# Kernel optimization log

Hardware: AMD Instinct MI355X
Metric: run time of the kernel (lower is better)

Reference implementation:

```python
import jax, jax.numpy as jnp
import numpy as np

OUTPUT_SIZES = [1, 3, 6, 8]  # SPP pyramid -> total KV length 110

def _bounds(n, out):
    # PyTorch AdaptiveMaxPool2d bin boundaries
    return [((i * n) // out, -((-(i + 1) * n) // out)) for i in range(out)]

def adaptive_max_pool2d(x, out):
    # x: [B, C, H, W] -> [B, C, out, out]
    B, C, H, W = x.shape
    rows = jnp.stack([x[:, :, s:e, :].max(axis=2) for s, e in _bounds(H, out)], axis=2)
    return jnp.stack([rows[:, :, :, s:e].max(axis=3) for s, e in _bounds(W, out)], axis=3)

def spp(x):
    # [B, C, H, W] -> [B, C, S] with S = sum(o*o) = 110
    B, C = x.shape[:2]
    return jnp.concatenate(
        [adaptive_max_pool2d(x, o).reshape(B, C, o * o) for o in OUTPUT_SIZES], axis=2)

def conv1x1(x, w):
    # 1x1 conv, no bias: w [O, C], x [B, C, H, W]
    return jnp.einsum('oc,bchw->bohw', w, x)

def setup_inputs() -> dict:
    key = jax.random.key(0)
    ks = jax.random.split(key, 6)
    B, C, H, W = 16, 512, 64, 64
    IC = C // 2
    x = jax.random.normal(ks[0], (B, C, H, W), jnp.float32)
    y = jax.random.normal(ks[1], (B, C, H, W), jnp.float32)
    sc = 1.0 / np.sqrt(C)
    w_phi = jax.random.normal(ks[2], (IC, C), jnp.float32) * sc
    w_theta = jax.random.normal(ks[3], (IC, C), jnp.float32) * sc
    w_g = jax.random.normal(ks[4], (IC, C), jnp.float32) * sc
    w_mask = jax.random.normal(ks[5], (C, IC), jnp.float32) * (1.0 / np.sqrt(IC))
    return {"x": x, "y": y, "w_phi": w_phi, "w_theta": w_theta,
            "w_g": w_g, "w_mask": w_mask}

def reference(x, y, w_phi, w_theta, w_g, w_mask):
    B, C, H, W = x.shape
    IC = w_phi.shape[0]
    N = H * W
    # Query: [B, N, IC]
    x_phi = conv1x1(x, w_phi).reshape(B, IC, N).transpose(0, 2, 1)
    # Keys/values from SPP-pooled y: [B, IC, S] / [B, S, IC]
    y_theta = spp(conv1x1(y, w_theta))
    y_g = spp(conv1x1(y, w_g)).transpose(0, 2, 1)
    # Attention with softmax over the QUERY axis (dim=1), as in the source
    attn = jax.nn.softmax(jnp.einsum('bnc,bcs->bns', x_phi, y_theta), axis=1)
    agg = jnp.einsum('bns,bsc->bnc', attn, y_g)          # [B, N, IC]
    agg = agg.transpose(0, 2, 1).reshape(B, IC, H, W)     # [B, IC, H, W]
    mask = conv1x1(agg, w_mask)                           # [B, C, H, W]
    return mask + x
```

## Files before the change

kernel.cpp:

```cpp
#include <hip/hip_runtime.h>

#define DI __device__ __forceinline__

typedef __attribute__((ext_vector_type(8))) __bf16 bf16x8;
typedef __attribute__((ext_vector_type(4))) float f32x4;

DI unsigned short f2bf(float x) {
  union { float f; unsigned u; } v; v.f = x;
  unsigned r = v.u + 0x7fffu + ((v.u >> 16) & 1u);
  return (unsigned short)(r >> 16);
}
DI float bf2f(unsigned short h) {
  union { unsigned u; float f; } v; v.u = ((unsigned)h) << 16;
  return v.f;
}
DI unsigned pack2(float a, float b) {
  return (unsigned)f2bf(a) | (((unsigned)f2bf(b)) << 16);
}

DI void gl_lds16(const void* g, void* l) {
  __builtin_amdgcn_global_load_lds(
      (const __attribute__((address_space(1))) void*)g,
      (__attribute__((address_space(3))) void*)l, 16, 0, 0);
}

__global__ __launch_bounds__(256) void pw_conv(
    const float* __restrict__ w_theta, const float* __restrict__ w_g,
    unsigned short* __restrict__ wTG)
{
  int e = (blockIdx.x * 256 + threadIdx.x) * 8;
  const float* src = (e < 131072) ? (w_theta + e) : (w_g + (e - 131072));
  float4 a = *(const float4*)src;
  float4 c = *(const float4*)(src + 4);
  uint4 u;
  u.x = pack2(a.x, a.y); u.y = pack2(a.z, a.w);
  u.z = pack2(c.x, c.y); u.w = pack2(c.z, c.w);
  *(uint4*)(wTG + e) = u;
}

__global__ __launch_bounds__(256) void p0_transpose(
    const float* __restrict__ src, unsigned short* __restrict__ dst)
{
  const int n0 = blockIdx.x * 64, c0 = blockIdx.y * 64, b = blockIdx.z;
  const int tid = threadIdx.x;
  __shared__ float T[64 * 65];
  #pragma unroll
  for (int p = 0; p < 4; ++p) {
    int r = p * 16 + (tid >> 4);
    int n4 = (tid & 15) << 2;
    *(float4*)&T[r * 65 + n4] =
        *(const float4*)(src + ((size_t)(b * 512 + c0 + r)) * 4096 + n0 + n4);
  }
  __syncthreads();
  int n = tid >> 2, cc = (tid & 3) * 16;
  unsigned u[8];
  #pragma unroll
  for (int j = 0; j < 16; j += 2)
    u[j >> 1] = pack2(T[(cc + j) * 65 + n], T[(cc + j + 1) * 65 + n]);
  unsigned short* d = dst + ((size_t)(b * 4096 + n0 + n)) * 512 + c0 + cc;
  *(uint4*)(d) = make_uint4(u[0], u[1], u[2], u[3]);
  *(uint4*)(d + 8) = make_uint4(u[4], u[5], u[6], u[7]);
}

__constant__ int c_RS[18] = {0, 0,21,42, 0,10,21,32,42,53, 0,8,16,24,32,40,48,56};
__constant__ int c_RE[18] = {64, 22,43,64, 11,22,32,43,54,64, 8,16,24,32,40,48,56,64};

__global__ __launch_bounds__(256) void k1f_conv_pool(
    const unsigned short* __restrict__ yT, const unsigned short* __restrict__ wTG,
    unsigned short* __restrict__ Rbuf)
{
  const int tid = threadIdx.x;
  const int id = blockIdx.x;
  const int tile = (id & 7) * 16 + (id >> 3);
  const int mb = (tile & 3) * 128;
  const int nbt = tile >> 2;
  const int nb = nbt * 128;
  const int b  = blockIdx.y;
  const int lane = tid & 63, wv = tid >> 6;
  const int wm = (wv & 1) * 64, wn = (wv >> 1) * 64;
  const int l15 = lane & 15, l4 = lane >> 4;

  __shared__ __align__(16) char smem[33280];
  unsigned short* As = (unsigned short*)smem;
  unsigned short* Bs = (unsigned short*)(smem + 8192);
  float* P = (float*)smem;

  f32x4 acc[4][4];
  #pragma unroll
  for (int i = 0; i < 4; ++i)
    #pragma unroll
    for (int j = 0; j < 4; ++j) acc[i][j] = f32x4{0.f, 0.f, 0.f, 0.f};

  for (int kb = 0; kb < 512; kb += 32) {
    #pragma unroll
    for (int p = 0; p < 2; ++p) {
      int chunk = (wv * 2 + p) * 64 + lane;
      int row = chunk >> 2, c16 = chunk & 3;
      gl_lds16(wTG + ((size_t)(mb + row)) * 512 + kb + c16 * 8,
               As + (wv * 2 + p) * 512);
      gl_lds16(yT + ((size_t)(b * 4096 + nb + row)) * 512 + kb + c16 * 8,
               Bs + (wv * 2 + p) * 512);
    }
    __syncthreads();
    bf16x8 af[4], bfr[4];
    #pragma unroll
    for (int i = 0; i < 4; ++i)
      af[i] = *(const bf16x8*)&As[(wm + i * 16 + l15) * 32 + l4 * 8];
    #pragma unroll
    for (int j = 0; j < 4; ++j)
      bfr[j] = *(const bf16x8*)&Bs[(wn + j * 16 + l15) * 32 + l4 * 8];
    #pragma unroll
    for (int i = 0; i < 4; ++i)
      #pragma unroll
      for (int j = 0; j < 4; ++j)
        acc[i][j] = __builtin_amdgcn_mfma_f32_16x16x32_bf16(af[i], bfr[j], acc[i][j], 0, 0, 0);
    __syncthreads();
  }

  const int hloc = wv >> 1;
  #pragma unroll
  for (int pass = 0; pass < 2; ++pass) {
    __syncthreads();
    if (hloc == pass) {
      #pragma unroll
      for (int i = 0; i < 4; ++i)
        #pragma unroll
        for (int j = 0; j < 4; ++j)
          #pragma unroll
          for (int r = 0; r < 4; ++r)
            P[(wm + i * 16 + l4 * 4 + r) * 65 + j * 16 + l15] = acc[i][j][r];
    }
    __syncthreads();
    const int o = tid & 127;
    size_t rbase = (((size_t)(b * 64 + nbt * 2 + pass)) * 18) * 512 + mb + o;
    if (tid < 128) {
      float b0 = -3.4e38f, b1 = b0, b2 = b0, b3 = b0;
      #pragma unroll
      for (int w = 0; w < 64; ++w) {
        float v = P[o * 65 + w];
        b0 = fmaxf(b0, v);
        if (w < 22) b1 = fmaxf(b1, v);
        if (w >= 21 && w < 43) b2 = fmaxf(b2, v);
        if (w >= 42) b3 = fmaxf(b3, v);
      }
      Rbuf[rbase]           = f2bf(b0);
      Rbuf[rbase + 512]     = f2bf(b1);
      Rbuf[rbase + 2 * 512] = f2bf(b2);
      Rbuf[rbase + 3 * 512] = f2bf(b3);
    } else {
      float s6[6], s8[8];
      #pragma unroll
      for (int i = 0; i < 6; ++i) s6[i] = -3.4e38f;
      #pragma unroll
      for (int i = 0; i < 8; ++i) s8[i] = -3.4e38f;
      constexpr int R6S[6] = {0, 10, 21, 32, 42, 53};
      constexpr int R6E[6] = {11, 22, 32, 43, 54, 64};
      #pragma unroll
      for (int w = 0; w < 64; ++w) {
        float v = P[o * 65 + w];
        #pragma unroll
        for (int i = 0; i < 6; ++i)
          if (w >= R6S[i] && w < R6E[i]) s6[i] = fmaxf(s6[i], v);
        s8[w >> 3] = fmaxf(s8[w >> 3], v);
      }
      #pragma unroll
      for (int i = 0; i < 6; ++i) Rbuf[rbase + (size_t)(4 + i) * 512] = f2bf(s6[i]);
      #pragma unroll
      for (int i = 0; i < 8; ++i) Rbuf[rbase + (size_t)(10 + i) * 512] = f2bf(s8[i]);
    }
  }
}

__global__ __launch_bounds__(256) void k2_pool_final(
    const unsigned short* __restrict__ Rbuf, float* __restrict__ Pt,
    float* __restrict__ Pg)
{
  const int s = blockIdx.x, b = blockIdx.y, tid = threadIdx.x;
  size_t obase = ((size_t)(b * 128) + s) * 256 + tid;
  if (s >= 110) { Pt[obase] = 0.f; Pg[obase] = 0.f; return; }
  int he, wb;
  if (s == 0)      { he = 0; wb = 0; }
  else if (s < 10) { int i = s - 1;  he = 1 + i / 3;  wb = 1 + i % 3; }
  else if (s < 46) { int i = s - 10; he = 4 + i / 6;  wb = 4 + i % 6; }
  else             { int i = s - 46; he = 10 + i / 8; wb = 10 + i % 8; }
  float m0 = -3.4e38f, m1 = -3.4e38f;
  int e = c_RE[he];
  for (int h = c_RS[he]; h < e; ++h) {
    const unsigned short* r = Rbuf + (((size_t)(b * 64 + h)) * 18 + wb) * 512;
    m0 = fmaxf(m0, bf2f(r[tid]));
    m1 = fmaxf(m1, bf2f(r[tid + 256]));
  }
  Pt[obase] = m0;
  Pg[obase] = m1;
}

__global__ __launch_bounds__(256) void k3_fused(
    const float* __restrict__ Pt, const float* __restrict__ Pg,
    const float* __restrict__ w_phi, const float* __restrict__ w_mask,
    unsigned short* __restrict__ Kth, unsigned short* __restrict__ Ktl,
    unsigned short* __restrict__ Vb)
{
  __shared__ __align__(16) char sm3[51200];
  const int tid = threadIdx.x;
  const int tx = tid & 15, ty = tid >> 4;
  const int b = blockIdx.y;
  if (blockIdx.z == 0) {
    const int ct = blockIdx.x;
    const int c0 = tx * 4, s0 = ty * 8;
    float* Ls = (float*)sm3;
    float* Ws = Ls + 128 * 64;
    float acc[8][4] = {};
    for (int kc = 0; kc < 256; kc += 64) {
      #pragma unroll
      for (int j = 0; j < 8; ++j) {
        int flat = tid + 256 * j;
        int row = flat >> 4, k4 = (flat & 15) << 2;
        *(float4*)&Ls[row * 64 + k4] =
            *(const float4*)(Pt + ((size_t)(b * 128) + row) * 256 + kc + k4);
      }
      #pragma unroll
      for (int j = 0; j < 4; ++j) {
        int flat = tid + 256 * j;
        int row = flat >> 4, c4 = (flat & 15) << 2;
        *(float4*)&Ws[row * 68 + c4] =
            *(const float4*)(w_phi + (size_t)(kc + row) * 512 + ct * 64 + c4);
      }
      __syncthreads();
      for (int k = 0; k < 64; k += 4) {
        float4 wv[4];
        #pragma unroll
        for (int kk = 0; kk < 4; ++kk) wv[kk] = *(const float4*)&Ws[(k + kk) * 68 + c0];
        #pragma unroll
        for (int i = 0; i < 8; ++i) {
          float4 a = *(const float4*)&Ls[(s0 + i) * 64 + k];
          const float* ap = (const float*)&a;
          #pragma unroll
          for (int kk = 0; kk < 4; ++kk) {
            const float* wp = (const float*)&wv[kk];
            acc[i][0] += ap[kk] * wp[0];
            acc[i][1] += ap[kk] * wp[1];
            acc[i][2] += ap[kk] * wp[2];
            acc[i][3] += ap[kk] * wp[3];
          }
        }
      }
      __syncthreads();
    }
    #pragma unroll
    for (int i = 0; i < 8; ++i) {
      unsigned short hi[4]; float lo[4];
      #pragma unroll
      for (int j = 0; j < 4; ++j) { hi[j] = f2bf(acc[i][j]); lo[j] = acc[i][j] - bf2f(hi[j]); }
      size_t base = ((size_t)(b * 128) + s0 + i) * 512 + ct * 64 + c0;
      uint2 uh; uh.x = (unsigned)hi[0] | ((unsigned)hi[1] << 16);
      uh.y = (unsigned)hi[2] | ((unsigned)hi[3] << 16);
      uint2 ul; ul.x = pack2(lo[0], lo[1]); ul.y = pack2(lo[2], lo[3]);
      *(uint2*)&Kth[base] = uh;
      *(uint2*)&Ktl[base] = ul;
    }
  } else {
    const int ot = blockIdx.x;
    const int o0 = ty * 4;
    float* Ws = (float*)sm3;
    float* Ps = Ws + 64 * 64;
    float acc[4][8] = {};
    for (int kc = 0; kc < 256; kc += 64) {
      #pragma unroll
      for (int j = 0; j < 4; ++j) {
        int flat = tid + 256 * j;
        int row = flat >> 4, k4 = (flat & 15) << 2;
        *(float4*)&Ws[row * 64 + k4] =
            *(const float4*)(w_mask + (size_t)(ot * 64 + row) * 256 + kc + k4);
      }
      #pragma unroll
      for (int j = 0; j < 8; ++j) {
        int flat = tid + 256 * j;
        int row = flat >> 4, k4 = (flat & 15) << 2;
        *(float4*)&Ps[row * 68 + k4] =
            *(const float4*)(Pg + ((size_t)(b * 128) + row) * 256 + kc + k4);
      }
      __syncthreads();
      for (int k = 0; k < 64; k += 4) {
        float4 wv[4];
        #pragma unroll
        for (int i = 0; i < 4; ++i) wv[i] = *(const float4*)&Ws[(o0 + i) * 64 + k];
        #pragma unroll
        for (int jj = 0; jj < 8; ++jj) {
          float4 pv = *(const float4*)&Ps[(tx + 16 * jj) * 68 + k];
          const float* pp = (const float*)&pv;
          #pragma unroll
          for (int i = 0; i < 4; ++i) {
            const float* wp = (const float*)&wv[i];
            #pragma unroll
            for (int kk = 0; kk < 4; ++kk) acc[i][jj] += wp[kk] * pp[kk];
          }
        }
      }
      __syncthreads();
    }
    #pragma unroll
    for (int i = 0; i < 4; ++i)
      #pragma unroll
      for (int jj = 0; jj < 8; ++jj)
        Vb[((size_t)(b * 512) + ot * 64 + o0 + i) * 128 + tx + 16 * jj] =
            f2bf(acc[i][jj]);
  }
}

__global__ __launch_bounds__(256) void k4_scores(
    const unsigned short* __restrict__ xT, const unsigned short* __restrict__ Kth,
    const unsigned short* __restrict__ Ktl, float* __restrict__ scores)
{
  const int tid = threadIdx.x;
  const int nb = blockIdx.x * 128;
  const int b = blockIdx.y;
  const int lane = tid & 63, wv = tid >> 6;
  const int wm = (wv & 1) * 64, wn = (wv >> 1) * 64;
  const int l15 = lane & 15, l4 = lane >> 4;
  __shared__ __align__(16) unsigned short Ah[128 * 32];
  __shared__ __align__(16) unsigned short Al[128 * 32];
  __shared__ __align__(16) unsigned short Bs[128 * 32];
  f32x4 acc[4][4];
  #pragma unroll
  for (int i = 0; i < 4; ++i)
    #pragma unroll
    for (int j = 0; j < 4; ++j) acc[i][j] = f32x4{0.f, 0.f, 0.f, 0.f};

  for (int kb = 0; kb < 512; kb += 32) {
    #pragma unroll
    for (int p = 0; p < 2; ++p) {
      int chunk = (wv * 2 + p) * 64 + lane;
      int row = chunk >> 2, c16 = chunk & 3;
      size_t g = ((size_t)(b * 128) + row) * 512 + kb + c16 * 8;
      gl_lds16(Kth + g, Ah + (wv * 2 + p) * 512);
      gl_lds16(Ktl + g, Al + (wv * 2 + p) * 512);
      gl_lds16(xT + ((size_t)(b * 4096 + nb + row)) * 512 + kb + c16 * 8,
               Bs + (wv * 2 + p) * 512);
    }
    __syncthreads();
    bf16x8 ah[4], al[4], bfr[4];
    #pragma unroll
    for (int i = 0; i < 4; ++i) {
      ah[i] = *(const bf16x8*)&Ah[(wm + i * 16 + l15) * 32 + l4 * 8];
      al[i] = *(const bf16x8*)&Al[(wm + i * 16 + l15) * 32 + l4 * 8];
    }
    #pragma unroll
    for (int j = 0; j < 4; ++j)
      bfr[j] = *(const bf16x8*)&Bs[(wn + j * 16 + l15) * 32 + l4 * 8];
    #pragma unroll
    for (int i = 0; i < 4; ++i)
      #pragma unroll
      for (int j = 0; j < 4; ++j) {
        acc[i][j] = __builtin_amdgcn_mfma_f32_16x16x32_bf16(ah[i], bfr[j], acc[i][j], 0, 0, 0);
        acc[i][j] = __builtin_amdgcn_mfma_f32_16x16x32_bf16(al[i], bfr[j], acc[i][j], 0, 0, 0);
      }
    __syncthreads();
  }
  #pragma unroll
  for (int i = 0; i < 4; ++i)
    #pragma unroll
    for (int j = 0; j < 4; ++j)
      #pragma unroll
      for (int r = 0; r < 4; ++r)
        scores[((size_t)(b * 128) + wm + i * 16 + l4 * 4 + r) * 4096 + nb + wn + j * 16 + l15] =
            acc[i][j][r];
}

__global__ __launch_bounds__(256) void k5_stats(
    const float* __restrict__ scores, float* __restrict__ mbuf,
    float* __restrict__ lbuf)
{
  const int s = blockIdx.x, b = blockIdx.y, tid = threadIdx.x;
  if (s >= 110) {
    if (tid == 0) { mbuf[b * 128 + s] = 0.f; lbuf[b * 128 + s] = 0.f; }
    return;
  }
  const float* row = scores + ((size_t)(b * 128) + s) * 4096;
  float4 v[4];
  float m = -3.4e38f;
  #pragma unroll
  for (int j = 0; j < 4; ++j) {
    v[j] = *(const float4*)(row + (tid + 256 * j) * 4);
    m = fmaxf(m, fmaxf(fmaxf(v[j].x, v[j].y), fmaxf(v[j].z, v[j].w)));
  }
  #pragma unroll
  for (int off = 32; off > 0; off >>= 1) m = fmaxf(m, __shfl_down(m, off));
  __shared__ float red[8];
  if ((tid & 63) == 0) red[tid >> 6] = m;
  __syncthreads();
  float mm = fmaxf(fmaxf(red[0], red[1]), fmaxf(red[2], red[3]));
  float sum = 0.f;
  #pragma unroll
  for (int j = 0; j < 4; ++j)
    sum += __expf(v[j].x - mm) + __expf(v[j].y - mm) +
           __expf(v[j].z - mm) + __expf(v[j].w - mm);
  #pragma unroll
  for (int off = 32; off > 0; off >>= 1) sum += __shfl_down(sum, off);
  if ((tid & 63) == 0) red[4 + (tid >> 6)] = sum;
  __syncthreads();
  if (tid == 0) {
    float S = red[4] + red[5] + red[6] + red[7];
    mbuf[b * 128 + s] = mm;
    lbuf[b * 128 + s] = 1.f / S;
  }
}

__global__ __launch_bounds__(256) void k5e_expT(
    const float* __restrict__ scores, const float* __restrict__ mbuf,
    const float* __restrict__ lbuf, unsigned short* __restrict__ Eb)
{
  const int nt = blockIdx.x, b = blockIdx.y, tid = threadIdx.x;
  __shared__ float L[128 * 68];
  __shared__ float sm[128], sl[128];
  if (tid < 128) { sm[tid] = mbuf[b * 128 + tid]; sl[tid] = lbuf[b * 128 + tid]; }
  #pragma unroll
  for (int j = 0; j < 8; ++j) {
    int flat = tid + 256 * j;
    int s = flat >> 4, n4 = (flat & 15) << 2;
    *(float4*)&L[s * 68 + n4] =
        *(const float4*)(scores + ((size_t)(b * 128) + s) * 4096 + nt * 64 + n4);
  }
  __syncthreads();
  int n = tid >> 2, sq = (tid & 3) * 32;
  unsigned ub[16];
  #pragma unroll
  for (int k = 0; k < 32; k += 2) {
    float e0 = __expf(L[(sq + k) * 68 + n] - sm[sq + k]) * sl[sq + k];
    float e1 = __expf(L[(sq + k + 1) * 68 + n] - sm[sq + k + 1]) * sl[sq + k + 1];
    ub[k >> 1] = pack2(e0, e1);
  }
  uint4* dst = (uint4*)(Eb + ((size_t)(b * 4096) + nt * 64 + n) * 128 + sq);
  #pragma unroll
  for (int j = 0; j < 4; ++j)
    dst[j] = make_uint4(ub[4 * j], ub[4 * j + 1], ub[4 * j + 2], ub[4 * j + 3]);
}

__global__ __launch_bounds__(256) void k6_out(
    const unsigned short* __restrict__ Eb, const unsigned short* __restrict__ Vb,
    const float* __restrict__ x, float* __restrict__ out)
{
  const int tid = threadIdx.x;
  const int nb = blockIdx.x * 128;
  const int mb = blockIdx.y * 128;
  const int b = blockIdx.z;
  const int lane = tid & 63, wv = tid >> 6;
  const int wm = (wv & 1) * 64, wn = (wv >> 1) * 64;
  const int l15 = lane & 15, l4 = lane >> 4;
  __shared__ __align__(16) unsigned short A0[128 * 32];
  __shared__ __align__(16) unsigned short A1[128 * 32];
  __shared__ __align__(16) unsigned short B0[128 * 32];
  __shared__ __align__(16) unsigned short B1[128 * 32];

  f32x4 acc[4][4];
  #pragma unroll
  for (int i = 0; i < 4; ++i)
    #pragma unroll
    for (int j = 0; j < 4; ++j) acc[i][j] = f32x4{0.f, 0.f, 0.f, 0.f};

  for (int kc = 0; kc < 128; kc += 64) {
    #pragma unroll
    for (int p = 0; p < 2; ++p) {
      int chunk = (wv * 2 + p) * 64 + lane;
      int row = chunk >> 2, c16 = chunk & 3;
      size_t ga = ((size_t)(b * 512) + mb + row) * 128 + kc + c16 * 8;
      gl_lds16(Vb + ga,      A0 + (wv * 2 + p) * 512);
      gl_lds16(Vb + ga + 32, A1 + (wv * 2 + p) * 512);
      size_t gb = ((size_t)(b * 4096) + nb + row) * 128 + kc + c16 * 8;
      gl_lds16(Eb + gb,      B0 + (wv * 2 + p) * 512);
      gl_lds16(Eb + gb + 32, B1 + (wv * 2 + p) * 512);
    }
    __syncthreads();
    #pragma unroll
    for (int h = 0; h < 2; ++h) {
      const unsigned short* Ak = h ? A1 : A0;
      const unsigned short* Bk = h ? B1 : B0;
      bf16x8 af[4], bfr[4];
      #pragma unroll
      for (int i = 0; i < 4; ++i)
        af[i] = *(const bf16x8*)&Ak[(wm + i * 16 + l15) * 32 + l4 * 8];
      #pragma unroll
      for (int j = 0; j < 4; ++j)
        bfr[j] = *(const bf16x8*)&Bk[(wn + j * 16 + l15) * 32 + l4 * 8];
      #pragma unroll
      for (int i = 0; i < 4; ++i)
        #pragma unroll
        for (int j = 0; j < 4; ++j)
          acc[i][j] = __builtin_amdgcn_mfma_f32_16x16x32_bf16(af[i], bfr[j], acc[i][j], 0, 0, 0);
    }
    __syncthreads();
  }
  #pragma unroll
  for (int i = 0; i < 4; ++i)
    #pragma unroll
    for (int j = 0; j < 4; ++j)
      #pragma unroll
      for (int r = 0; r < 4; ++r) {
        int o = mb + wm + i * 16 + l4 * 4 + r;
        size_t idx = ((size_t)(b * 512) + o) * 4096 + nb + wn + j * 16 + l15;
        out[idx] = acc[i][j][r] + x[idx];
      }
}

extern "C" void kernel_launch(void* const* d_in, const int* in_sizes, int n_in,
                              void* d_out, int out_size, void* d_ws, size_t ws_size,
                              hipStream_t stream)
{
  (void)in_sizes; (void)n_in; (void)out_size; (void)ws_size;
  const float* x       = (const float*)d_in[0];
  const float* y       = (const float*)d_in[1];
  const float* w_phi   = (const float*)d_in[2];
  const float* w_theta = (const float*)d_in[3];
  const float* w_g     = (const float*)d_in[4];
  const float* w_mask  = (const float*)d_in[5];
  float* out = (float*)d_out;

  char* ws = (char*)d_ws;
  unsigned short* yT = (unsigned short*)ws;
  unsigned short* xT = yT;
  char* B0 = ws + 67108864;
  unsigned short* Rbuf = (unsigned short*)B0;
  float* scores = (float*)B0;
  unsigned short* Eb = (unsigned short*)(B0 + 33554432);
  unsigned short* wTG = (unsigned short*)(B0 + 50331648);
  unsigned short* Vb  = (unsigned short*)(B0 + 50331648);
  char* C0 = B0 + 54525952;
  float* Pt = (float*)C0;
  float* Pg = (float*)(C0 + 2097152);
  unsigned short* Kth = (unsigned short*)(C0 + 4194304);
  unsigned short* Ktl = (unsigned short*)(C0 + 6291456);
  float* mbuf = (float*)(C0 + 8388608);
  float* lbuf = (float*)(C0 + 8396800);

  pw_conv<<<dim3(128), 256, 0, stream>>>(w_theta, w_g, wTG);
  p0_transpose<<<dim3(64, 8, 16), 256, 0, stream>>>(y, yT);
  k1f_conv_pool<<<dim3(128, 16), 256, 0, stream>>>(yT, wTG, Rbuf);
  k2_pool_final<<<dim3(128, 16), 256, 0, stream>>>(Rbuf, Pt, Pg);
  k3_fused<<<dim3(8, 16, 2), 256, 0, stream>>>(Pt, Pg, w_phi, w_mask, Kth, Ktl, Vb);
  p0_transpose<<<dim3(64, 8, 16), 256, 0, stream>>>(x, xT);
  k4_scores<<<dim3(32, 16), 256, 0, stream>>>(xT, Kth, Ktl, scores);
  k5_stats<<<dim3(128, 16), 256, 0, stream>>>(scores, mbuf, lbuf);
  k5e_expT<<<dim3(64, 16), 256, 0, stream>>>(scores, mbuf, lbuf, Eb);
  k6_out<<<dim3(32, 4, 16), 256, 0, stream>>>(Eb, Vb, x, out);
}
```

Measured before the change: 521.4 us.

## Fuse weight cast into transpose, double-buffer GEMMs, fold softmax stats into scores

Several independent changes. The weight bf16 conversion now runs as extra blocks of the y transpose launch. k1 and k4 use double-buffered LDS staging so the next K-slice loads during MFMA. k4 computes per-tile partial max and sum-exp for the query-axis softmax, which removes the k5_stats pass that re-read the whole scores tensor; k5e merges the 32 partials per row. k6 loads the full K=128 slice in one stage and prefetches the residual x before the MFMAs. The costs are more LDS per block, which may lower occupancy, and a small extra partial-statistics buffer.

Measured after the change: 501.3 us. -3.9%, faster.

```diff
diff --git a/kernel.cpp b/kernel.cpp
--- a/kernel.cpp
+++ b/kernel.cpp
@@ -24,23 +24,24 @@
       (__attribute__((address_space(3))) void*)l, 16, 0, 0);
 }
 
-__global__ __launch_bounds__(256) void pw_conv(
+__global__ __launch_bounds__(256) void p0w_transpose(
+    const float* __restrict__ src, unsigned short* __restrict__ dst,
     const float* __restrict__ w_theta, const float* __restrict__ w_g,
     unsigned short* __restrict__ wTG)
 {
-  int e = (blockIdx.x * 256 + threadIdx.x) * 8;
-  const float* src = (e < 131072) ? (w_theta + e) : (w_g + (e - 131072));
-  float4 a = *(const float4*)src;
-  float4 c = *(const float4*)(src + 4);
-  uint4 u;
-  u.x = pack2(a.x, a.y); u.y = pack2(a.z, a.w);
-  u.z = pack2(c.x, c.y); u.w = pack2(c.z, c.w);
-  *(uint4*)(wTG + e) = u;
-}
-
-__global__ __launch_bounds__(256) void p0_transpose(
-    const float* __restrict__ src, unsigned short* __restrict__ dst)
-{
+  if (blockIdx.z == 16) {
+    if (blockIdx.y < 2) {
+      int e = ((blockIdx.y * 64 + blockIdx.x) * 256 + threadIdx.x) * 8;
+      const float* s = (e < 131072) ? (w_theta + e) : (w_g + (e - 131072));
+      float4 a = *(const float4*)s;
+      float4 c = *(const float4*)(s + 4);
+      uint4 u;
+      u.x = pack2(a.x, a.y); u.y = pack2(a.z, a.w);
+      u.z = pack2(c.x, c.y); u.w = pack2(c.z, c.w);
+      *(uint4*)(wTG + e) = u;
+    }
+    return;
+  }
   const int n0 = blockIdx.x * 64, c0 = blockIdx.y * 64, b = blockIdx.z;
   const int tid = threadIdx.x;
   __shared__ float T[64 * 65];
@@ -81,8 +82,6 @@
   const int l15 = lane & 15, l4 = lane >> 4;
 
   __shared__ __align__(16) char smem[33280];
-  unsigned short* As = (unsigned short*)smem;
-  unsigned short* Bs = (unsigned short*)(smem + 8192);
   float* P = (float*)smem;
 
   f32x4 acc[4][4];
@@ -91,7 +90,9 @@
     #pragma unroll
     for (int j = 0; j < 4; ++j) acc[i][j] = f32x4{0.f, 0.f, 0.f, 0.f};
 
-  for (int kb = 0; kb < 512; kb += 32) {
+  auto stage = [&](int buf, int kb) {
+    unsigned short* As = (unsigned short*)(smem + buf * 16384);
+    unsigned short* Bs = As + 4096;
     #pragma unroll
     for (int p = 0; p < 2; ++p) {
       int chunk = (wv * 2 + p) * 64 + lane;
@@ -101,7 +102,15 @@
       gl_lds16(yT + ((size_t)(b * 4096 + nb + row)) * 512 + kb + c16 * 8,
                Bs + (wv * 2 + p) * 512);
     }
-    __syncthreads();
+  };
+
+  stage(0, 0);
+  __syncthreads();
+  int cur = 0;
+  for (int t = 0; t < 16; ++t) {
+    if (t < 15) stage(cur ^ 1, (t + 1) * 32);
+    const unsigned short* As = (const unsigned short*)(smem + cur * 16384);
+    const unsigned short* Bs = As + 4096;
     bf16x8 af[4], bfr[4];
     #pragma unroll
     for (int i = 0; i < 4; ++i)
@@ -115,6 +124,7 @@
       for (int j = 0; j < 4; ++j)
         acc[i][j] = __builtin_amdgcn_mfma_f32_16x16x32_bf16(af[i], bfr[j], acc[i][j], 0, 0, 0);
     __syncthreads();
+    cur ^= 1;
   }
 
   const int hloc = wv >> 1;
@@ -309,24 +319,28 @@
 
 __global__ __launch_bounds__(256) void k4_scores(
     const unsigned short* __restrict__ xT, const unsigned short* __restrict__ Kth,
-    const unsigned short* __restrict__ Ktl, float* __restrict__ scores)
+    const unsigned short* __restrict__ Ktl, float* __restrict__ scores,
+    float* __restrict__ pmax_g, float* __restrict__ psum_g)
 {
   const int tid = threadIdx.x;
-  const int nb = blockIdx.x * 128;
+  const int ntile = blockIdx.x;
+  const int nb = ntile * 128;
   const int b = blockIdx.y;
   const int lane = tid & 63, wv = tid >> 6;
   const int wm = (wv & 1) * 64, wn = (wv >> 1) * 64;
   const int l15 = lane & 15, l4 = lane >> 4;
-  __shared__ __align__(16) unsigned short Ah[128 * 32];
-  __shared__ __align__(16) unsigned short Al[128 * 32];
-  __shared__ __align__(16) unsigned short Bs[128 * 32];
+  __shared__ __align__(16) char smem4[49152];
+  __shared__ float SmP[256], SsP[256];
   f32x4 acc[4][4];
   #pragma unroll
   for (int i = 0; i < 4; ++i)
     #pragma unroll
     for (int j = 0; j < 4; ++j) acc[i][j] = f32x4{0.f, 0.f, 0.f, 0.f};
 
-  for (int kb = 0; kb < 512; kb += 32) {
+  auto stage = [&](int buf, int kb) {
+    unsigned short* Ah = (unsigned short*)(smem4 + buf * 24576);
+    unsigned short* Al = Ah + 4096;
+    unsigned short* Bs = Al + 4096;
     #pragma unroll
     for (int p = 0; p < 2; ++p) {
       int chunk = (wv * 2 + p) * 64 + lane;
@@ -337,7 +351,16 @@
       gl_lds16(xT + ((size_t)(b * 4096 + nb + row)) * 512 + kb + c16 * 8,
                Bs + (wv * 2 + p) * 512);
     }
-    __syncthreads();
+  };
+
+  stage(0, 0);
+  __syncthreads();
+  int cur = 0;
+  for (int t = 0; t < 16; ++t) {
+    if (t < 15) stage(cur ^ 1, (t + 1) * 32);
+    const unsigned short* Ah = (const unsigned short*)(smem4 + cur * 24576);
+    const unsigned short* Al = Ah + 4096;
+    const unsigned short* Bs = Al + 4096;
     bf16x8 ah[4], al[4], bfr[4];
     #pragma unroll
     for (int i = 0; i < 4; ++i) {
@@ -355,7 +378,9 @@
         acc[i][j] = __builtin_amdgcn_mfma_f32_16x16x32_bf16(al[i], bfr[j], acc[i][j], 0, 0, 0);
       }
     __syncthreads();
-  }
+    cur ^= 1;
+  }
+
   #pragma unroll
   for (int i = 0; i < 4; ++i)
     #pragma unroll
@@ -364,55 +389,71 @@
       for (int r = 0; r < 4; ++r)
         scores[((size_t)(b * 128) + wm + i * 16 + l4 * 4 + r) * 4096 + nb + wn + j * 16 + l15] =
             acc[i][j][r];
-}
-
-__global__ __launch_bounds__(256) void k5_stats(
-    const float* __restrict__ scores, float* __restrict__ mbuf,
-    float* __restrict__ lbuf)
-{
-  const int s = blockIdx.x, b = blockIdx.y, tid = threadIdx.x;
-  if (s >= 110) {
-    if (tid == 0) { mbuf[b * 128 + s] = 0.f; lbuf[b * 128 + s] = 0.f; }
-    return;
-  }
-  const float* row = scores + ((size_t)(b * 128) + s) * 4096;
-  float4 v[4];
-  float m = -3.4e38f;
-  #pragma unroll
-  for (int j = 0; j < 4; ++j) {
-    v[j] = *(const float4*)(row + (tid + 256 * j) * 4);
-    m = fmaxf(m, fmaxf(fmaxf(v[j].x, v[j].y), fmaxf(v[j].z, v[j].w)));
-  }
-  #pragma unroll
-  for (int off = 32; off > 0; off >>= 1) m = fmaxf(m, __shfl_down(m, off));
-  __shared__ float red[8];
-  if ((tid & 63) == 0) red[tid >> 6] = m;
-  __syncthreads();
-  float mm = fmaxf(fmaxf(red[0], red[1]), fmaxf(red[2], red[3]));
-  float sum = 0.f;
-  #pragma unroll
-  for (int j = 0; j < 4; ++j)
-    sum += __expf(v[j].x - mm) + __expf(v[j].y - mm) +
-           __expf(v[j].z - mm) + __expf(v[j].w - mm);
-  #pragma unroll
-  for (int off = 32; off > 0; off >>= 1) sum += __shfl_down(sum, off);
-  if ((tid & 63) == 0) red[4 + (tid >> 6)] = sum;
-  __syncthreads();
-  if (tid == 0) {
-    float S = red[4] + red[5] + red[6] + red[7];
-    mbuf[b * 128 + s] = mm;
-    lbuf[b * 128 + s] = 1.f / S;
+
+  const int nh = wn >> 6;
+  float cm[4][4];
+  #pragma unroll
+  for (int i = 0; i < 4; ++i)
+    #pragma unroll
+    for (int r = 0; r < 4; ++r) {
+      float v = fmaxf(fmaxf(acc[i][0][r], acc[i][1][r]),
+                      fmaxf(acc[i][2][r], acc[i][3][r]));
+      v = fmaxf(v, __shfl_xor(v, 1));
+      v = fmaxf(v, __shfl_xor(v, 2));
+      v = fmaxf(v, __shfl_xor(v, 4));
+      v = fmaxf(v, __shfl_xor(v, 8));
+      if (l15 == 0) SmP[(wm + i * 16 + l4 * 4 + r) * 2 + nh] = v;
+    }
+  __syncthreads();
+  #pragma unroll
+  for (int i = 0; i < 4; ++i)
+    #pragma unroll
+    for (int r = 0; r < 4; ++r) {
+      int s = wm + i * 16 + l4 * 4 + r;
+      cm[i][r] = fmaxf(SmP[s * 2], SmP[s * 2 + 1]);
+    }
+  #pragma unroll
+  for (int i = 0; i < 4; ++i)
+    #pragma unroll
+    for (int r = 0; r < 4; ++r) {
+      float s0 = __expf(acc[i][0][r] - cm[i][r]) + __expf(acc[i][1][r] - cm[i][r]) +
+                 __expf(acc[i][2][r] - cm[i][r]) + __expf(acc[i][3][r] - cm[i][r]);
+      s0 += __shfl_xor(s0, 1);
+      s0 += __shfl_xor(s0, 2);
+      s0 += __shfl_xor(s0, 4);
+      s0 += __shfl_xor(s0, 8);
+      if (l15 == 0) SsP[(wm + i * 16 + l4 * 4 + r) * 2 + nh] = s0;
+    }
+  __syncthreads();
+  if (tid < 128) {
+    size_t pidx = ((size_t)(b * 128) + tid) * 32 + ntile;
+    pmax_g[pidx] = fmaxf(SmP[tid * 2], SmP[tid * 2 + 1]);
+    psum_g[pidx] = SsP[tid * 2] + SsP[tid * 2 + 1];
   }
 }
 
 __global__ __launch_bounds__(256) void k5e_expT(
-    const float* __restrict__ scores, const float* __restrict__ mbuf,
-    const float* __restrict__ lbuf, unsigned short* __restrict__ Eb)
+    const float* __restrict__ scores, const float* __restrict__ pmax_g,
+    const float* __restrict__ psum_g, unsigned short* __restrict__ Eb)
 {
   const int nt = blockIdx.x, b = blockIdx.y, tid = threadIdx.x;
   __shared__ float L[128 * 68];
   __shared__ float sm[128], sl[128];
-  if (tid < 128) { sm[tid] = mbuf[b * 128 + tid]; sl[tid] = lbuf[b * 128 + tid]; }
+  if (tid < 128) {
+    float M = 0.f, linv = 0.f;
+    if (tid < 110) {
+      const float* pm = pmax_g + ((size_t)(b * 128) + tid) * 32;
+      const float* ps = psum_g + ((size_t)(b * 128) + tid) * 32;
+      M = -3.4e38f;
+      #pragma unroll
+      for (int t = 0; t < 32; ++t) M = fmaxf(M, pm[t]);
+      float S = 0.f;
+      #pragma unroll
+      for (int t = 0; t < 32; ++t) S += ps[t] * __expf(pm[t] - M);
+      linv = 1.f / S;
+    }
+    sm[tid] = M; sl[tid] = linv;
+  }
   #pragma unroll
   for (int j = 0; j < 8; ++j) {
     int flat = tid + 256 * j;
@@ -446,48 +487,52 @@
   const int lane = tid & 63, wv = tid >> 6;
   const int wm = (wv & 1) * 64, wn = (wv >> 1) * 64;
   const int l15 = lane & 15, l4 = lane >> 4;
-  __shared__ __align__(16) unsigned short A0[128 * 32];
-  __shared__ __align__(16) unsigned short A1[128 * 32];
-  __shared__ __align__(16) unsigned short B0[128 * 32];
-  __shared__ __align__(16) unsigned short B1[128 * 32];
-
-  f32x4 acc[4][4];
-  #pragma unroll
-  for (int i = 0; i < 4; ++i)
-    #pragma unroll
-    for (int j = 0; j < 4; ++j) acc[i][j] = f32x4{0.f, 0.f, 0.f, 0.f};
-
-  for (int kc = 0; kc < 128; kc += 64) {
+  __shared__ __align__(16) unsigned short SA[4][4096];
+  __shared__ __align__(16) unsigned short SB[4][4096];
+
+  #pragma unroll
+  for (int h = 0; h < 4; ++h)
     #pragma unroll
     for (int p = 0; p < 2; ++p) {
       int chunk = (wv * 2 + p) * 64 + lane;
       int row = chunk >> 2, c16 = chunk & 3;
-      size_t ga = ((size_t)(b * 512) + mb + row) * 128 + kc + c16 * 8;
-      gl_lds16(Vb + ga,      A0 + (wv * 2 + p) * 512);
-      gl_lds16(Vb + ga + 32, A1 + (wv * 2 + p) * 512);
-      size_t gb = ((size_t)(b * 4096) + nb + row) * 128 + kc + c16 * 8;
-      gl_lds16(Eb + gb,      B0 + (wv * 2 + p) * 512);
-      gl_lds16(Eb + gb + 32, B1 + (wv * 2 + p) * 512);
-    }
-    __syncthreads();
-    #pragma unroll
-    for (int h = 0; h < 2; ++h) {
-      const unsigned short* Ak = h ? A1 : A0;
-      const unsigned short* Bk = h ? B1 : B0;
-      bf16x8 af[4], bfr[4];
-      #pragma unroll
-      for (int i = 0; i < 4; ++i)
-        af[i] = *(const bf16x8*)&Ak[(wm + i * 16 + l15) * 32 + l4 * 8];
+      gl_lds16(Vb + ((size_t)(b * 512) + mb + row) * 128 + h * 32 + c16 * 8,
+               &SA[h][(wv * 2 + p) * 512]);
+      gl_lds16(Eb + ((size_t)(b * 4096) + nb + row) * 128 + h * 32 + c16 * 8,
+               &SB[h][(wv * 2 + p) * 512]);
+    }
+
+  float xr[4][4][4];
+  #pragma unroll
+  for (int i = 0; i < 4; ++i)
+    #pragma unroll
+    for (int j = 0; j < 4; ++j)
+      #pragma unroll
+      for (int r = 0; r < 4; ++r)
+        xr[i][j][r] = x[((size_t)(b * 512) + mb + wm + i * 16 + l4 * 4 + r) * 4096 +
+                        nb + wn + j * 16 + l15];
+
+  f32x4 acc[4][4];
+  #pragma unroll
+  for (int i = 0; i < 4; ++i)
+    #pragma unroll
+    for (int j = 0; j < 4; ++j) acc[i][j] = f32x4{0.f, 0.f, 0.f, 0.f};
+
+  __syncthreads();
+  #pragma unroll
+  for (int h = 0; h < 4; ++h) {
+    bf16x8 af[4], bfr[4];
+    #pragma unroll
+    for (int i = 0; i < 4; ++i)
+      af[i] = *(const bf16x8*)&SA[h][(wm + i * 16 + l15) * 32 + l4 * 8];
+    #pragma unroll
+    for (int j = 0; j < 4; ++j)
+      bfr[j] = *(const bf16x8*)&SB[h][(wn + j * 16 + l15) * 32 + l4 * 8];
+    #pragma unroll
+    for (int i = 0; i < 4; ++i)
       #pragma unroll
       for (int j = 0; j < 4; ++j)
-        bfr[j] = *(const bf16x8*)&Bk[(wn + j * 16 + l15) * 32 + l4 * 8];
-      #pragma unroll
-      for (int i = 0; i < 4; ++i)
-        #pragma unroll
-        for (int j = 0; j < 4; ++j)
-          acc[i][j] = __builtin_amdgcn_mfma_f32_16x16x32_bf16(af[i], bfr[j], acc[i][j], 0, 0, 0);
-    }
-    __syncthreads();
+        acc[i][j] = __builtin_amdgcn_mfma_f32_16x16x32_bf16(af[i], bfr[j], acc[i][j], 0, 0, 0);
   }
   #pragma unroll
   for (int i = 0; i < 4; ++i)
@@ -497,7 +542,7 @@
       for (int r = 0; r < 4; ++r) {
         int o = mb + wm + i * 16 + l4 * 4 + r;
         size_t idx = ((size_t)(b * 512) + o) * 4096 + nb + wn + j * 16 + l15;
-        out[idx] = acc[i][j][r] + x[idx];
+        out[idx] = acc[i][j][r] + xr[i][j][r];
       }
 }
 
@@ -523,22 +568,20 @@
   unsigned short* Eb = (unsigned short*)(B0 + 33554432);
   unsigned short* wTG = (unsigned short*)(B0 + 50331648);
   unsigned short* Vb  = (unsigned short*)(B0 + 50331648);
+  float* pmax_g = (float*)(B0 + 52428800);
+  float* psum_g = (float*)(B0 + 52690944);
   char* C0 = B0 + 54525952;
   float* Pt = (float*)C0;
   float* Pg = (float*)(C0 + 2097152);
   unsigned short* Kth = (unsigned short*)(C0 + 4194304);
   unsigned short* Ktl = (unsigned short*)(C0 + 6291456);
-  float* mbuf = (float*)(C0 + 8388608);
-  float* lbuf = (float*)(C0 + 8396800);
-
-  pw_conv<<<dim3(128), 256, 0, stream>>>(w_theta, w_g, wTG);
-  p0_transpose<<<dim3(64, 8, 16), 256, 0, stream>>>(y, yT);
+
+  p0w_transpose<<<dim3(64, 8, 17), 256, 0, stream>>>(y, yT, w_theta, w_g, wTG);
   k1f_conv_pool<<<dim3(128, 16), 256, 0, stream>>>(yT, wTG, Rbuf);
   k2_pool_final<<<dim3(128, 16), 256, 0, stream>>>(Rbuf, Pt, Pg);
   k3_fused<<<dim3(8, 16, 2), 256, 0, stream>>>(Pt, Pg, w_phi, w_mask, Kth, Ktl, Vb);
-  p0_transpose<<<dim3(64, 8, 16), 256, 0, stream>>>(x, xT);
-  k4_scores<<<dim3(32, 16), 256, 0, stream>>>(xT, Kth, Ktl, scores);
-  k5_stats<<<dim3(128, 16), 256, 0, stream>>>(scores, mbuf, lbuf);
-  k5e_expT<<<dim3(64, 16), 256, 0, stream>>>(scores, mbuf, lbuf, Eb);
+  p0w_transpose<<<dim3(64, 8, 16), 256, 0, stream>>>(x, xT, w_theta, w_g, wTG);
+  k4_scores<<<dim3(32, 16), 256, 0, stream>>>(xT, Kth, Ktl, scores, pmax_g, psum_g);
+  k5e_expT<<<dim3(64, 16), 256, 0, stream>>>(scores, pmax_g, psum_g, Eb);
   k6_out<<<dim3(32, 4, 16), 256, 0, stream>>>(Eb, Vb, x, out);
 }
```
